# Kernel tuning notes

Hardware: AMD Instinct MI355X
Metric: run time of the kernel (lower is better)

Reference implementation:

```python
import jax, jax.numpy as jnp
import numpy as np

N = 100000
E = 1600000
F_IN = 128
H1, C1 = 8, 8          # conv1: heads=8, hidden_channels=8 -> concat dim 64
H2, C2 = 1, 40         # conv2: heads=1, out=num_classes=40, concat=False
NEG_SLOPE = 0.2
EPS = 1e-16


def setup_inputs() -> dict:
    key = jax.random.key(0)
    ks = jax.random.split(key, 10)
    x = jax.random.normal(ks[0], (N, F_IN), dtype=jnp.float32)
    edge_index = jax.random.randint(ks[1], (2, E), 0, N, dtype=jnp.int32)
    s1 = 1.0 / np.sqrt(F_IN)
    s2 = 1.0 / np.sqrt(H1 * C1)
    W1 = jax.random.normal(ks[2], (F_IN, H1 * C1), dtype=jnp.float32) * s1
    att_src1 = jax.random.normal(ks[3], (H1, C1), dtype=jnp.float32) * s2
    att_dst1 = jax.random.normal(ks[4], (H1, C1), dtype=jnp.float32) * s2
    b1 = jnp.zeros((H1 * C1,), dtype=jnp.float32)
    W2 = jax.random.normal(ks[5], (H1 * C1, H2 * C2), dtype=jnp.float32) * s2
    att_src2 = jax.random.normal(ks[6], (H2, C2), dtype=jnp.float32) * (1.0 / np.sqrt(C2))
    att_dst2 = jax.random.normal(ks[7], (H2, C2), dtype=jnp.float32) * (1.0 / np.sqrt(C2))
    b2 = jnp.zeros((C2,), dtype=jnpp_zeros_dtype()) if False else jnp.zeros((C2,), dtype=jnp.float32)
    return {"x": x, "W1": W1, "att_src1": att_src1, "att_dst1": att_dst1, "b1": b1,
            "W2": W2, "att_src2": att_src2, "att_dst2": att_dst2, "b2": b2,
            "edge_index": edge_index}


def _gat_conv(x, W, att_src, att_dst, bias, src, dst, num_nodes, concat):
    """PyG GATConv (eval mode, self-loops already added to src/dst)."""
    H, C = att_src.shape
    h = (x @ W).reshape(num_nodes, H, C)                 # [N, H, C]
    a_src = jnp.sum(h * att_src[None], axis=-1)          # [N, H]
    a_dst = jnp.sum(h * att_dst[None], axis=-1)          # [N, H]
    e = a_src[src] + a_dst[dst]                          # [Etot, H]
    e = jax.nn.leaky_relu(e, NEG_SLOPE)
    # segment softmax over incoming edges of each dst node
    e_max = jax.ops.segment_max(e, dst, num_segments=num_nodes)   # [N, H]
    ex = jnp.exp(e - e_max[dst])
    denom = jax.ops.segment_sum(ex, dst, num_segments=num_nodes)  # [N, H]
    alpha = ex / (denom[dst] + EPS)                      # [Etot, H]
    msg = h[src] * alpha[..., None]                      # [Etot, H, C]
    out = jax.ops.segment_sum(msg, dst, num_segments=num_nodes)   # [N, H, C]
    if concat:
        out = out.reshape(num_nodes, H * C)
    else:
        out = out.mean(axis=1)
    return out + bias


def reference(x, W1, att_src1, att_dst1, b1, W2, att_src2, att_dst2, b2, edge_index):
    # add self-loops (PyG GATConv default add_self_loops=True)
    loops = jnp.arange(N, dtype=edge_index.dtype)
    src = jnp.concatenate([edge_index[0], loops])
    dst = jnp.concatenate([edge_index[1], loops])
    # dropout layers are identity in eval mode
    emb = jax.nn.elu(_gat_conv(x, W1, att_src1, att_dst1, b1, src, dst, N, True))
    logits = _gat_conv(emb, W2, att_src2, att_dst2, b2, src, dst, N, False)
    return jax.nn.log_softmax(logits, axis=1), emb


def jnp_zeros_dtype():
    return jnp.float32
```

## Files before the change

### kernel.cpp

```cpp
#include <hip/hip_runtime.h>
#include <hip/hip_fp16.h>
#include <math.h>

#define NN 100000
#define EE 1600000
#define ET (EE + NN)
#define FIN 128
#define D1 64
#define H1 8
#define C1 8
#define C2 40
#define NEG 0.2f
#define EPSV 1e-16f
#define LOG2E 1.4426950408889634f

#define NBKT 196
#define BCAP 10240
#define CHUNK 8192
#define NBB ((ET + CHUNK - 1) / CHUNK)
#define H2S 48

__device__ __forceinline__ void edge_sd(int e, const int* __restrict__ ei, int& s, int& d) {
  if (e < EE) { s = ei[e]; d = ei[EE + e]; }
  else        { s = e - EE; d = s; }
}

__global__ __launch_bounds__(256) void scatter_kernel(const int* __restrict__ ei,
                                                      int* __restrict__ gcur,
                                                      int* __restrict__ ecsr) {
  __shared__ int lh[NBKT], lres[NBKT], lcur[NBKT];
  int t = threadIdx.x;
  if (t < NBKT) { lh[t] = 0; lcur[t] = 0; }
  __syncthreads();
  int e0 = blockIdx.x * CHUNK;
  int e1 = min(e0 + CHUNK, ET);
  for (int e = e0 + t; e < e1; e += 256) {
    int d = (e < EE) ? ei[EE + e] : e - EE;
    atomicAdd(&lh[d >> 9], 1);
  }
  __syncthreads();
  if (t < NBKT && lh[t]) lres[t] = atomicAdd(&gcur[t], lh[t]);
  __syncthreads();
  for (int e = e0 + t; e < e1; e += 256) {
    int s, d; edge_sd(e, ei, s, d);
    int b = d >> 9;
    int lp = atomicAdd(&lcur[b], 1);
    ecsr[b * BCAP + lres[b] + lp] = s | ((d & 511) << 17);
  }
}

__global__ __launch_bounds__(256) void bucket2csr_kernel(const int* __restrict__ gcur,
                                                         int2* __restrict__ rowrng,
                                                         int* __restrict__ ecsr) {
  __shared__ int ebuf[BCAP];
  __shared__ int hist[512];
  __shared__ int sd[256];
  int b = blockIdx.x, t = threadIdx.x;
  int base = b * BCAP;
  int cnt = gcur[b];
  hist[t] = 0; hist[t + 256] = 0;
  __syncthreads();
  for (int i = t; i < cnt; i += 256) {
    int p = ecsr[base + i];
    ebuf[i] = p;
    atomicAdd(&hist[p >> 17], 1);
  }
  __syncthreads();
  int h0 = hist[2 * t], h1 = hist[2 * t + 1], s = h0 + h1;
  sd[t] = s;
  __syncthreads();
  for (int off = 1; off < 256; off <<= 1) {
    int x = sd[t];
    int y = (t >= off) ? sd[t - off] : 0;
    __syncthreads();
    sd[t] = x + y;
    __syncthreads();
  }
  int run = sd[t] - s;
  int g = b * 512 + 2 * t;
  if (g < NN)     rowrng[g]     = make_int2(base + run,      base + run + h0);
  if (g + 1 < NN) rowrng[g + 1] = make_int2(base + run + h0, base + run + h0 + h1);
  hist[2 * t] = run;
  hist[2 * t + 1] = run + h0;
  __syncthreads();
  for (int i = t; i < cnt; i += 256) {
    int p = ebuf[i];
    int pos = atomicAdd(&hist[p >> 17], 1);
    ecsr[base + pos] = p & 0x1FFFF;
  }
}

__global__ __launch_bounds__(256) void gemm1_kernel(
    const float* __restrict__ x, const float* __restrict__ W,
    const float* __restrict__ att_s, const float* __restrict__ att_d,
    __half* __restrict__ h, float* __restrict__ as, float* __restrict__ ad) {
  __shared__ float sW[FIN * D1];
  __shared__ float sx[64 * FIN];
  int t = threadIdx.x;
  int node0 = blockIdx.x * 64;
  {
    const float4* Wg = (const float4*)W;
    float4* sWq = (float4*)sW;
    for (int i = t; i < FIN * D1 / 4; i += 256) sWq[i] = Wg[i];
  }
  for (int idx = t; idx < 64 * 32; idx += 256) {
    int node = idx >> 5, kq = idx & 31;
    float4 v = make_float4(0.f, 0.f, 0.f, 0.f);
    if (node0 + node < NN) v = ((const float4*)x)[(size_t)(node0 + node) * 32 + kq];
    *(float4*)&sx[node * FIN + ((kq * 4 + 4 * (node >> 2)) & 127)] = v;
  }
  __syncthreads();
  int lane = t & 63, wid = t >> 6;
  int ng = lane & 15, cgl = lane >> 4;
  int col0 = wid * 16 + cgl * 4;
  float acc[4][4];
#pragma unroll
  for (int a = 0; a < 4; ++a)
#pragma unroll
    for (int c = 0; c < 4; ++c) acc[a][c] = 0.f;
  for (int kk = 0; kk < FIN; kk += 4) {
    float4 xv[4], wv[4];
#pragma unroll
    for (int a = 0; a < 4; ++a) {
      int node = ng * 4 + a;
      xv[a] = *(const float4*)&sx[node * FIN + ((kk + 4 * (node >> 2)) & 127)];
    }
#pragma unroll
    for (int b = 0; b < 4; ++b) wv[b] = *(const float4*)&sW[(kk + b) * D1 + col0];
#pragma unroll
    for (int a = 0; a < 4; ++a) {
      acc[a][0] = fmaf(xv[a].x, wv[0].x, acc[a][0]);
      acc[a][1] = fmaf(xv[a].x, wv[0].y, acc[a][1]);
      acc[a][2] = fmaf(xv[a].x, wv[0].z, acc[a][2]);
      acc[a][3] = fmaf(xv[a].x, wv[0].w, acc[a][3]);
      acc[a][0] = fmaf(xv[a].y, wv[1].x, acc[a][0]);
      acc[a][1] = fmaf(xv[a].y, wv[1].y, acc[a][1]);
      acc[a][2] = fmaf(xv[a].y, wv[1].z, acc[a][2]);
      acc[a][3] = fmaf(xv[a].y, wv[1].w, acc[a][3]);
      acc[a][0] = fmaf(xv[a].z, wv[2].x, acc[a][0]);
      acc[a][1] = fmaf(xv[a].z, wv[2].y, acc[a][1]);
      acc[a][2] = fmaf(xv[a].z, wv[2].z, acc[a][2]);
      acc[a][3] = fmaf(xv[a].z, wv[2].w, acc[a][3]);
      acc[a][0] = fmaf(xv[a].w, wv[3].x, acc[a][0]);
      acc[a][1] = fmaf(xv[a].w, wv[3].y, acc[a][1]);
      acc[a][2] = fmaf(xv[a].w, wv[3].z, acc[a][2]);
      acc[a][3] = fmaf(xv[a].w, wv[3].w, acc[a][3]);
    }
  }
#pragma unroll
  for (int a = 0; a < 4; ++a) {
    int node = node0 + ng * 4 + a;
    if (node < NN) {
      __half2 p01 = __floats2half2_rn(acc[a][0], acc[a][1]);
      __half2 p23 = __floats2half2_rn(acc[a][2], acc[a][3]);
      __half2* hp = (__half2*)&h[(size_t)node * D1 + col0];
      hp[0] = p01; hp[1] = p23;
    }
  }
  float aw_s[4], aw_d[4];
#pragma unroll
  for (int j = 0; j < 4; ++j) {
    aw_s[j] = att_s[col0 + j] * LOG2E;
    aw_d[j] = att_d[col0 + j] * LOG2E;
  }
#pragma unroll
  for (int a = 0; a < 4; ++a) {
    float ps = acc[a][0]*aw_s[0] + acc[a][1]*aw_s[1] + acc[a][2]*aw_s[2] + acc[a][3]*aw_s[3];
    float pd = acc[a][0]*aw_d[0] + acc[a][1]*aw_d[1] + acc[a][2]*aw_d[2] + acc[a][3]*aw_d[3];
    ps += __shfl_xor(ps, 16, 64);
    pd += __shfl_xor(pd, 16, 64);
    int node = node0 + ng * 4 + a;
    if ((cgl & 1) == 0 && node < NN) {
      int head = 2 * wid + (cgl >> 1);
      as[node * H1 + head] = ps;
      ad[node * H1 + head] = pd;
    }
  }
}

__global__ __launch_bounds__(256) void agg1_kernel(
    const int2* __restrict__ rowrng, const int* __restrict__ csr,
    const float* __restrict__ as, const float* __restrict__ ad,
    const __half* __restrict__ h, const float* __restrict__ b1,
    float* __restrict__ emb) {
  int t = threadIdx.x;
  int lane = t & 63;
  int o = lane >> 3;
  int k = lane & 7;
  int ob = lane & 56;
  int node = blockIdx.x * 32 + (t >> 6) * 8 + o;
  int2 rr = rowrng[node];
  int beg = rr.x, deg = rr.y - rr.x, degm1 = deg - 1;
  float adv = ad[node * H1 + k];
  float den = 0.f;
  float a0=0.f,a1=0.f,a2=0.f,a3=0.f,a4=0.f,a5=0.f,a6=0.f,a7=0.f;
  int sreg = csr[beg + min(k, degm1)];
  for (int i = 0; i < deg; i += 8) {
    int snext = csr[beg + min(i + 8 + k, degm1)];
#pragma unroll
    for (int r = 0; r < 8; ++r) {
      int sj = __shfl(sreg, ob + r, 64);
      uint4 u = *(const uint4*)(h + ((size_t)(uint)sj << 6) + (k << 3));
      float av = as[(uint)sj * 8u + k];
      float xx = av + adv; xx = fmaxf(xx, NEG * xx);
      float e = (i + r < deg) ? exp2f(xx) : 0.f;
      den += e;
      float2 f;
      f = __half22float2(*(__half2*)&u.x); a0 = fmaf(f.x, e, a0); a1 = fmaf(f.y, e, a1);
      f = __half22float2(*(__half2*)&u.y); a2 = fmaf(f.x, e, a2); a3 = fmaf(f.y, e, a3);
      f = __half22float2(*(__half2*)&u.z); a4 = fmaf(f.x, e, a4); a5 = fmaf(f.y, e, a5);
      f = __half22float2(*(__half2*)&u.w); a6 = fmaf(f.x, e, a6); a7 = fmaf(f.y, e, a7);
    }
    sreg = snext;
  }
  float4 bv0 = ((const float4*)b1)[2 * k];
  float4 bv1 = ((const float4*)b1)[2 * k + 1];
  float inv = 1.0f / (den + EPSV);
  float v0 = fmaf(a0, inv, bv0.x), v1 = fmaf(a1, inv, bv0.y);
  float v2 = fmaf(a2, inv, bv0.z), v3 = fmaf(a3, inv, bv0.w);
  float v4 = fmaf(a4, inv, bv1.x), v5 = fmaf(a5, inv, bv1.y);
  float v6 = fmaf(a6, inv, bv1.z), v7 = fmaf(a7, inv, bv1.w);
  v0 = v0 > 0.f ? v0 : expm1f(v0); v1 = v1 > 0.f ? v1 : expm1f(v1);
  v2 = v2 > 0.f ? v2 : expm1f(v2); v3 = v3 > 0.f ? v3 : expm1f(v3);
  v4 = v4 > 0.f ? v4 : expm1f(v4); v5 = v5 > 0.f ? v5 : expm1f(v5);
  v6 = v6 > 0.f ? v6 : expm1f(v6); v7 = v7 > 0.f ? v7 : expm1f(v7);
  float4 s0; s0.x = v0; s0.y = v1; s0.z = v2; s0.w = v3;
  float4 s1; s1.x = v4; s1.y = v5; s1.z = v6; s1.w = v7;
  float* ep = emb + (size_t)node * D1 + (k << 3);
  ((float4*)ep)[0] = s0; ((float4*)ep)[1] = s1;
}

__global__ __launch_bounds__(256) void gemm2_kernel(
    const float* __restrict__ emb, const float* __restrict__ W2,
    const float* __restrict__ att_s, const float* __restrict__ att_d,
    __half* __restrict__ h2, float* __restrict__ ad) {
  __shared__ float sW[D1 * D1];
  __shared__ float se[64 * D1];
  __shared__ float sred_s[64], sred_d[64];
  int t = threadIdx.x;
  int node0 = blockIdx.x * 64;
  for (int i = t; i < D1 * D1; i += 256) {
    int k = i >> 6, c = i & 63;
    sW[i] = (c < C2) ? W2[k * C2 + c] : 0.f;
  }
  for (int idx = t; idx < 64 * 16; idx += 256) {
    int node = idx >> 4, kq = idx & 15;
    float4 v = make_float4(0.f, 0.f, 0.f, 0.f);
    if (node0 + node < NN) v = ((const float4*)emb)[(size_t)(node0 + node) * 16 + kq];
    *(float4*)&se[node * D1 + ((kq * 4 + 4 * (node >> 2)) & 63)] = v;
  }
  if (t < 64) { sred_s[t] = 0.f; sred_d[t] = 0.f; }
  __syncthreads();
  int lane = t & 63, wid = t >> 6;
  int ng = lane & 15, cgl = lane >> 4;
  int col0 = wid * 16 + cgl * 4;
  float acc[4][4];
#pragma unroll
  for (int a = 0; a < 4; ++a)
#pragma unroll
    for (int c = 0; c < 4; ++c) acc[a][c] = 0.f;
  for (int kk = 0; kk < D1; kk += 4) {
    float4 xv[4], wv[4];
#pragma unroll
    for (int a = 0; a < 4; ++a) {
      int node = ng * 4 + a;
      xv[a] = *(const float4*)&se[node * D1 + ((kk + 4 * (node >> 2)) & 63)];
    }
#pragma unroll
    for (int b = 0; b < 4; ++b) wv[b] = *(const float4*)&sW[(kk + b) * D1 + col0];
#pragma unroll
    for (int a = 0; a < 4; ++a) {
      acc[a][0] = fmaf(xv[a].x, wv[0].x, acc[a][0]);
      acc[a][1] = fmaf(xv[a].x, wv[0].y, acc[a][1]);
      acc[a][2] = fmaf(xv[a].x, wv[0].z, acc[a][2]);
      acc[a][3] = fmaf(xv[a].x, wv[0].w, acc[a][3]);
      acc[a][0] = fmaf(xv[a].y, wv[1].x, acc[a][0]);
      acc[a][1] = fmaf(xv[a].y, wv[1].y, acc[a][1]);
      acc[a][2] = fmaf(xv[a].y, wv[1].z, acc[a][2]);
      acc[a][3] = fmaf(xv[a].y, wv[1].w, acc[a][3]);
      acc[a][0] = fmaf(xv[a].z, wv[2].x, acc[a][0]);
      acc[a][1] = fmaf(xv[a].z, wv[2].y, acc[a][1]);
      acc[a][2] = fmaf(xv[a].z, wv[2].z, acc[a][2]);
      acc[a][3] = fmaf(xv[a].z, wv[2].w, acc[a][3]);
      acc[a][0] = fmaf(xv[a].w, wv[3].x, acc[a][0]);
      acc[a][1] = fmaf(xv[a].w, wv[3].y, acc[a][1]);
      acc[a][2] = fmaf(xv[a].w, wv[3].z, acc[a][2]);
      acc[a][3] = fmaf(xv[a].w, wv[3].w, acc[a][3]);
    }
  }
  if (col0 < C2) {
#pragma unroll
    for (int a = 0; a < 4; ++a) {
      int node = node0 + ng * 4 + a;
      if (node < NN) {
        __half2 p01 = __floats2half2_rn(acc[a][0], acc[a][1]);
        __half2 p23 = __floats2half2_rn(acc[a][2], acc[a][3]);
        __half2* hp = (__half2*)&h2[(size_t)node * H2S + col0];
        hp[0] = p01; hp[1] = p23;
      }
    }
    float aw_s[4], aw_d[4];
#pragma unroll
    for (int j = 0; j < 4; ++j) {
      aw_s[j] = att_s[col0 + j] * LOG2E;
      aw_d[j] = att_d[col0 + j] * LOG2E;
    }
#pragma unroll
    for (int a = 0; a < 4; ++a) {
      float ps = acc[a][0]*aw_s[0] + acc[a][1]*aw_s[1] + acc[a][2]*aw_s[2] + acc[a][3]*aw_s[3];
      float pd = acc[a][0]*aw_d[0] + acc[a][1]*aw_d[1] + acc[a][2]*aw_d[2] + acc[a][3]*aw_d[3];
      atomicAdd(&sred_s[ng * 4 + a], ps);
      atomicAdd(&sred_d[ng * 4 + a], pd);
    }
  }
  __syncthreads();
  if (t < 64 && node0 + t < NN) {
    h2[(size_t)(node0 + t) * H2S + 40] = __float2half(sred_s[t]);
    ad[node0 + t] = sred_d[t];
  }
}

__global__ __launch_bounds__(256) void agg2_kernel(
    const int2* __restrict__ rowrng, const int* __restrict__ csr,
    const float* __restrict__ ad, const __half* __restrict__ h2,
    const float* __restrict__ b2, float* __restrict__ out) {
  int t = threadIdx.x;
  int lane = t & 63;
  int o = lane >> 3;
  int k = lane & 7;
  int ob = lane & 56;
  int kc = min(k, 4);
  int node = blockIdx.x * 32 + (t >> 6) * 8 + o;
  int2 rr = rowrng[node];
  int beg = rr.x, deg = rr.y - rr.x, degm1 = deg - 1;
  float adv = ad[node];
  float den = 0.f;
  float a0=0.f,a1=0.f,a2=0.f,a3=0.f,a4=0.f,a5=0.f,a6=0.f,a7=0.f;
  int sreg = csr[beg + min(k, degm1)];
  for (int i = 0; i < deg; i += 8) {
    int snext = csr[beg + min(i + 8 + k, degm1)];
#pragma unroll
    for (int r = 0; r < 8; ++r) {
      int sj = __shfl(sreg, ob + r, 64);
      const __half* rA = h2 + (size_t)(uint)sj * H2S;
      uint4 u = *(const uint4*)(rA + (kc << 3));
      float av = __half2float(rA[40]);
      float xx = av + adv; xx = fmaxf(xx, NEG * xx);
      float e = (i + r < deg) ? exp2f(xx) : 0.f;
      den += e;
      float2 f;
      f = __half22float2(*(__half2*)&u.x); a0 = fmaf(f.x, e, a0); a1 = fmaf(f.y, e, a1);
      f = __half22float2(*(__half2*)&u.y); a2 = fmaf(f.x, e, a2); a3 = fmaf(f.y, e, a3);
      f = __half22float2(*(__half2*)&u.z); a4 = fmaf(f.x, e, a4); a5 = fmaf(f.y, e, a5);
      f = __half22float2(*(__half2*)&u.w); a6 = fmaf(f.x, e, a6); a7 = fmaf(f.y, e, a7);
    }
    sreg = snext;
  }
  float4 bv0 = ((const float4*)b2)[2 * kc];
  float4 bv1 = ((const float4*)b2)[2 * kc + 1];
  float inv = 1.0f / (den + EPSV);
  float v0 = fmaf(a0, inv, bv0.x), v1 = fmaf(a1, inv, bv0.y);
  float v2 = fmaf(a2, inv, bv0.z), v3 = fmaf(a3, inv, bv0.w);
  float v4 = fmaf(a4, inv, bv1.x), v5 = fmaf(a5, inv, bv1.y);
  float v6 = fmaf(a6, inv, bv1.z), v7 = fmaf(a7, inv, bv1.w);
  bool act = (k < 5);
  float m = act ? fmaxf(fmaxf(fmaxf(v0, v1), fmaxf(v2, v3)),
                        fmaxf(fmaxf(v4, v5), fmaxf(v6, v7))) : -INFINITY;
#pragma unroll
  for (int off = 1; off < 8; off <<= 1) m = fmaxf(m, __shfl_xor(m, off, 64));
  float ex = act ? (__expf(v0 - m) + __expf(v1 - m) + __expf(v2 - m) + __expf(v3 - m) +
                    __expf(v4 - m) + __expf(v5 - m) + __expf(v6 - m) + __expf(v7 - m)) : 0.f;
#pragma unroll
  for (int off = 1; off < 8; off <<= 1) ex += __shfl_xor(ex, off, 64);
  if (act) {
    float lls = m + logf(ex);
    float4 s0; s0.x = v0 - lls; s0.y = v1 - lls; s0.z = v2 - lls; s0.w = v3 - lls;
    float4 s1; s1.x = v4 - lls; s1.y = v5 - lls; s1.z = v6 - lls; s1.w = v7 - lls;
    float* op = out + (size_t)node * C2 + (k << 3);
    ((float4*)op)[0] = s0; ((float4*)op)[1] = s1;
  }
}

extern "C" void kernel_launch(void* const* d_in, const int* in_sizes, int n_in,
                              void* d_out, int out_size, void* d_ws, size_t ws_size,
                              hipStream_t stream) {
  const float* x    = (const float*)d_in[0];
  const float* W1   = (const float*)d_in[1];
  const float* as1w = (const float*)d_in[2];
  const float* ad1w = (const float*)d_in[3];
  const float* b1   = (const float*)d_in[4];
  const float* W2   = (const float*)d_in[5];
  const float* as2w = (const float*)d_in[6];
  const float* ad2w = (const float*)d_in[7];
  const float* b2   = (const float*)d_in[8];
  const int*   ei   = (const int*)d_in[9];

  float* out   = (float*)d_out;
  float* outls = out;
  float* emb   = out + (long)NN * C2;

  char* wsb = (char*)d_ws;
  __half* h1   = (__half*)wsb; wsb += sizeof(__half) * (size_t)NN * D1;
  __half* h2   = (__half*)wsb; wsb += sizeof(__half) * ((size_t)NN * H2S + 64);
  float* asrc1 = (float*)wsb; wsb += sizeof(float) * (size_t)NN * H1;
  float* adst1 = (float*)wsb; wsb += sizeof(float) * (size_t)NN * H1;
  float* adst2 = (float*)wsb; wsb += sizeof(float) * (size_t)NN;
  int2* rowrng = (int2*)wsb;  wsb += sizeof(int2) * (size_t)NN;
  int* gcur    = (int*)wsb;   wsb += sizeof(int) * (NBKT + 4);
  int* ecsr    = (int*)wsb;   wsb += sizeof(int) * (size_t)NBKT * BCAP;

  hipMemsetAsync(gcur, 0, sizeof(int) * (NBKT + 4), stream);
  scatter_kernel<<<NBB, 256, 0, stream>>>(ei, gcur, ecsr);
  bucket2csr_kernel<<<NBKT, 256, 0, stream>>>(gcur, rowrng, ecsr);

  gemm1_kernel<<<(NN + 63) / 64, 256, 0, stream>>>(x, W1, as1w, ad1w, h1, asrc1, adst1);
  agg1_kernel<<<NN / 32, 256, 0, stream>>>(rowrng, ecsr, asrc1, adst1, h1, b1, emb);

  gemm2_kernel<<<(NN + 63) / 64, 256, 0, stream>>>(emb, W2, as2w, ad2w, h2, adst2);
  agg2_kernel<<<NN / 32, 256, 0, stream>>>(rowrng, ecsr, adst2, h2, b2, outls);
}
```

Before: 316.8 us.

## Use MFMA fp16 GEMMs with folded attention weights and double-buffered gathers

```diff
diff --git a/kernel.cpp b/kernel.cpp
--- a/kernel.cpp
+++ b/kernel.cpp
@@ -18,7 +18,9 @@
 #define BCAP 10240
 #define CHUNK 8192
 #define NBB ((ET + CHUNK - 1) / CHUNK)
-#define H2S 48
+
+typedef _Float16 f16x8 __attribute__((ext_vector_type(8)));
+typedef float f32x4 __attribute__((ext_vector_type(4)));
 
 __device__ __forceinline__ void edge_sd(int e, const int* __restrict__ ei, int& s, int& d) {
   if (e < EE) { s = ei[e]; d = ei[EE + e]; }
@@ -90,128 +92,142 @@
   }
 }
 
+__global__ __launch_bounds__(256) void prep_kernel(
+    const float* __restrict__ W1, const float* __restrict__ as1, const float* __restrict__ ad1,
+    const float* __restrict__ W2, const float* __restrict__ as2, const float* __restrict__ ad2w,
+    __half* __restrict__ Wf1, __half* __restrict__ Wf2) {
+  int gid = blockIdx.x * 256 + threadIdx.x;
+  int stride = gridDim.x * 256;
+  for (int idx = gid; idx < 4 * 5 * 64 * 8; idx += stride) {
+    int j = idx & 7, l = (idx >> 3) & 63;
+    int g = idx >> 9;
+    int ct = g % 5, kk = g / 5;
+    int kdim = kk * 32 + (l >> 4) * 8 + j;
+    int c = l & 15;
+    float v;
+    if (ct < 4) v = W1[kdim * 64 + ct * 16 + c];
+    else {
+      const float* aw = (c < 8) ? as1 : ad1;
+      int hh = c & 7;
+      float acc = 0.f;
+      for (int q = 0; q < 8; ++q) acc += W1[kdim * 64 + hh * 8 + q] * aw[hh * 8 + q];
+      v = acc * LOG2E;
+    }
+    Wf1[idx] = __float2half(v);
+  }
+  for (int idx = gid; idx < 2 * 3 * 64 * 8; idx += stride) {
+    int j = idx & 7, l = (idx >> 3) & 63;
+    int g = idx >> 9;
+    int ct = g % 3, kk = g / 3;
+    int kdim = kk * 32 + (l >> 4) * 8 + j;
+    int c = ct * 16 + (l & 15);
+    float v = 0.f;
+    if (c < C2) v = W2[kdim * C2 + c];
+    else if (c == 40 || c == 41) {
+      const float* aw = (c == 40) ? as2 : ad2w;
+      float acc = 0.f;
+      for (int q = 0; q < C2; ++q) acc += W2[kdim * C2 + q] * aw[q];
+      v = acc * LOG2E;
+    }
+    Wf2[idx] = __float2half(v);
+  }
+}
+
 __global__ __launch_bounds__(256) void gemm1_kernel(
-    const float* __restrict__ x, const float* __restrict__ W,
-    const float* __restrict__ att_s, const float* __restrict__ att_d,
-    __half* __restrict__ h, float* __restrict__ as, float* __restrict__ ad) {
-  __shared__ float sW[FIN * D1];
-  __shared__ float sx[64 * FIN];
+    const float* __restrict__ x, const __half* __restrict__ Wf1,
+    __half* __restrict__ h, __half* __restrict__ as_h, float* __restrict__ ad) {
   int t = threadIdx.x;
-  int node0 = blockIdx.x * 64;
-  {
-    const float4* Wg = (const float4*)W;
-    float4* sWq = (float4*)sW;
-    for (int i = t; i < FIN * D1 / 4; i += 256) sWq[i] = Wg[i];
-  }
-  for (int idx = t; idx < 64 * 32; idx += 256) {
-    int node = idx >> 5, kq = idx & 31;
-    float4 v = make_float4(0.f, 0.f, 0.f, 0.f);
-    if (node0 + node < NN) v = ((const float4*)x)[(size_t)(node0 + node) * 32 + kq];
-    *(float4*)&sx[node * FIN + ((kq * 4 + 4 * (node >> 2)) & 127)] = v;
-  }
-  __syncthreads();
-  int lane = t & 63, wid = t >> 6;
-  int ng = lane & 15, cgl = lane >> 4;
-  int col0 = wid * 16 + cgl * 4;
-  float acc[4][4];
-#pragma unroll
-  for (int a = 0; a < 4; ++a)
-#pragma unroll
-    for (int c = 0; c < 4; ++c) acc[a][c] = 0.f;
-  for (int kk = 0; kk < FIN; kk += 4) {
-    float4 xv[4], wv[4];
-#pragma unroll
-    for (int a = 0; a < 4; ++a) {
-      int node = ng * 4 + a;
-      xv[a] = *(const float4*)&sx[node * FIN + ((kk + 4 * (node >> 2)) & 127)];
-    }
-#pragma unroll
-    for (int b = 0; b < 4; ++b) wv[b] = *(const float4*)&sW[(kk + b) * D1 + col0];
-#pragma unroll
-    for (int a = 0; a < 4; ++a) {
-      acc[a][0] = fmaf(xv[a].x, wv[0].x, acc[a][0]);
-      acc[a][1] = fmaf(xv[a].x, wv[0].y, acc[a][1]);
-      acc[a][2] = fmaf(xv[a].x, wv[0].z, acc[a][2]);
-      acc[a][3] = fmaf(xv[a].x, wv[0].w, acc[a][3]);
-      acc[a][0] = fmaf(xv[a].y, wv[1].x, acc[a][0]);
-      acc[a][1] = fmaf(xv[a].y, wv[1].y, acc[a][1]);
-      acc[a][2] = fmaf(xv[a].y, wv[1].z, acc[a][2]);
-      acc[a][3] = fmaf(xv[a].y, wv[1].w, acc[a][3]);
-      acc[a][0] = fmaf(xv[a].z, wv[2].x, acc[a][0]);
-      acc[a][1] = fmaf(xv[a].z, wv[2].y, acc[a][1]);
-      acc[a][2] = fmaf(xv[a].z, wv[2].z, acc[a][2]);
-      acc[a][3] = fmaf(xv[a].z, wv[2].w, acc[a][3]);
-      acc[a][0] = fmaf(xv[a].w, wv[3].x, acc[a][0]);
-      acc[a][1] = fmaf(xv[a].w, wv[3].y, acc[a][1]);
-      acc[a][2] = fmaf(xv[a].w, wv[3].z, acc[a][2]);
-      acc[a][3] = fmaf(xv[a].w, wv[3].w, acc[a][3]);
-    }
-  }
-#pragma unroll
-  for (int a = 0; a < 4; ++a) {
-    int node = node0 + ng * 4 + a;
-    if (node < NN) {
-      __half2 p01 = __floats2half2_rn(acc[a][0], acc[a][1]);
-      __half2 p23 = __floats2half2_rn(acc[a][2], acc[a][3]);
-      __half2* hp = (__half2*)&h[(size_t)node * D1 + col0];
-      hp[0] = p01; hp[1] = p23;
-    }
-  }
-  float aw_s[4], aw_d[4];
-#pragma unroll
-  for (int j = 0; j < 4; ++j) {
-    aw_s[j] = att_s[col0 + j] * LOG2E;
-    aw_d[j] = att_d[col0 + j] * LOG2E;
-  }
-#pragma unroll
-  for (int a = 0; a < 4; ++a) {
-    float ps = acc[a][0]*aw_s[0] + acc[a][1]*aw_s[1] + acc[a][2]*aw_s[2] + acc[a][3]*aw_s[3];
-    float pd = acc[a][0]*aw_d[0] + acc[a][1]*aw_d[1] + acc[a][2]*aw_d[2] + acc[a][3]*aw_d[3];
-    ps += __shfl_xor(ps, 16, 64);
-    pd += __shfl_xor(pd, 16, 64);
-    int node = node0 + ng * 4 + a;
-    if ((cgl & 1) == 0 && node < NN) {
-      int head = 2 * wid + (cgl >> 1);
-      as[node * H1 + head] = ps;
-      ad[node * H1 + head] = pd;
-    }
-  }
-}
+  int w = t >> 6, lane = t & 63;
+  int col = lane & 15, kg = lane >> 4;
+  int node0 = blockIdx.x * 64 + w * 16;
+  int nodeA = min(node0 + col, NN - 1);
+  const float* xr = x + (size_t)nodeA * FIN + kg * 8;
+  const f16x8* Wq = (const f16x8*)Wf1;
+  f32x4 acc0 = {0.f,0.f,0.f,0.f}, acc1 = acc0, acc2 = acc0, acc3 = acc0, acc4 = acc0;
+#pragma unroll
+  for (int kk = 0; kk < 4; ++kk) {
+    float4 xa = *(const float4*)(xr + kk * 32);
+    float4 xb = *(const float4*)(xr + kk * 32 + 4);
+    f16x8 a;
+    a[0] = (_Float16)xa.x; a[1] = (_Float16)xa.y; a[2] = (_Float16)xa.z; a[3] = (_Float16)xa.w;
+    a[4] = (_Float16)xb.x; a[5] = (_Float16)xb.y; a[6] = (_Float16)xb.z; a[7] = (_Float16)xb.w;
+    acc0 = __builtin_amdgcn_mfma_f32_16x16x32_f16(a, Wq[(kk * 5 + 0) * 64 + lane], acc0, 0, 0, 0);
+    acc1 = __builtin_amdgcn_mfma_f32_16x16x32_f16(a, Wq[(kk * 5 + 1) * 64 + lane], acc1, 0, 0, 0);
+    acc2 = __builtin_amdgcn_mfma_f32_16x16x32_f16(a, Wq[(kk * 5 + 2) * 64 + lane], acc2, 0, 0, 0);
+    acc3 = __builtin_amdgcn_mfma_f32_16x16x32_f16(a, Wq[(kk * 5 + 3) * 64 + lane], acc3, 0, 0, 0);
+    acc4 = __builtin_amdgcn_mfma_f32_16x16x32_f16(a, Wq[(kk * 5 + 4) * 64 + lane], acc4, 0, 0, 0);
+  }
+#pragma unroll
+  for (int reg = 0; reg < 4; ++reg) {
+    int nr = node0 + kg * 4 + reg;
+    if (nr < NN) {
+      h[(size_t)nr * 64 +  0 + col] = __float2half(acc0[reg]);
+      h[(size_t)nr * 64 + 16 + col] = __float2half(acc1[reg]);
+      h[(size_t)nr * 64 + 32 + col] = __float2half(acc2[reg]);
+      h[(size_t)nr * 64 + 48 + col] = __float2half(acc3[reg]);
+      float v = acc4[reg];
+      if (col < 8) as_h[nr * 8 + col] = __float2half(v);
+      else         ad[nr * 8 + col - 8] = v;
+    }
+  }
+}
+
+#define CONS(u, avh, valid) do { \
+    float xx = __half2float(avh) + adv; xx = fmaxf(xx, NEG * xx); \
+    float e = (valid) ? exp2f(xx) : 0.f; den += e; \
+    float2 f; \
+    f = __half22float2(*(const __half2*)&(u).x); a0 = fmaf(f.x, e, a0); a1 = fmaf(f.y, e, a1); \
+    f = __half22float2(*(const __half2*)&(u).y); a2 = fmaf(f.x, e, a2); a3 = fmaf(f.y, e, a3); \
+    f = __half22float2(*(const __half2*)&(u).z); a4 = fmaf(f.x, e, a4); a5 = fmaf(f.y, e, a5); \
+    f = __half22float2(*(const __half2*)&(u).w); a6 = fmaf(f.x, e, a6); a7 = fmaf(f.y, e, a7); \
+  } while (0)
 
 __global__ __launch_bounds__(256) void agg1_kernel(
     const int2* __restrict__ rowrng, const int* __restrict__ csr,
-    const float* __restrict__ as, const float* __restrict__ ad,
+    const __half* __restrict__ as_h, const float* __restrict__ ad,
     const __half* __restrict__ h, const float* __restrict__ b1,
     float* __restrict__ emb) {
   int t = threadIdx.x;
   int lane = t & 63;
-  int o = lane >> 3;
-  int k = lane & 7;
-  int ob = lane & 56;
+  int o = lane >> 3, k = lane & 7, ob = lane & 56;
   int node = blockIdx.x * 32 + (t >> 6) * 8 + o;
   int2 rr = rowrng[node];
   int beg = rr.x, deg = rr.y - rr.x, degm1 = deg - 1;
-  float adv = ad[node * H1 + k];
+  float adv = ad[node * 8 + k];
   float den = 0.f;
   float a0=0.f,a1=0.f,a2=0.f,a3=0.f,a4=0.f,a5=0.f,a6=0.f,a7=0.f;
-  int sreg = csr[beg + min(k, degm1)];
-  for (int i = 0; i < deg; i += 8) {
-    int snext = csr[beg + min(i + 8 + k, degm1)];
+  uint4 uA[8]; __half vA[8]; int sjA[8];
+  int sA = csr[beg + min(k, degm1)];
+#pragma unroll
+  for (int r = 0; r < 8; ++r) sjA[r] = __shfl(sA, ob + r, 64);
+#pragma unroll
+  for (int r = 0; r < 8; ++r) {
+    uA[r] = *(const uint4*)(h + ((size_t)(uint)sjA[r] << 6) + (k << 3));
+    vA[r] = as_h[(uint)sjA[r] * 8u + k];
+  }
+  for (int i = 0; i < deg; i += 16) {
+    int sB = csr[beg + min(i + 8 + k, degm1)];
+    int sjB[8];
+#pragma unroll
+    for (int r = 0; r < 8; ++r) sjB[r] = __shfl(sB, ob + r, 64);
+    uint4 uB[8]; __half vB[8];
 #pragma unroll
     for (int r = 0; r < 8; ++r) {
-      int sj = __shfl(sreg, ob + r, 64);
-      uint4 u = *(const uint4*)(h + ((size_t)(uint)sj << 6) + (k << 3));
-      float av = as[(uint)sj * 8u + k];
-      float xx = av + adv; xx = fmaxf(xx, NEG * xx);
-      float e = (i + r < deg) ? exp2f(xx) : 0.f;
-      den += e;
-      float2 f;
-      f = __half22float2(*(__half2*)&u.x); a0 = fmaf(f.x, e, a0); a1 = fmaf(f.y, e, a1);
-      f = __half22float2(*(__half2*)&u.y); a2 = fmaf(f.x, e, a2); a3 = fmaf(f.y, e, a3);
-      f = __half22float2(*(__half2*)&u.z); a4 = fmaf(f.x, e, a4); a5 = fmaf(f.y, e, a5);
-      f = __half22float2(*(__half2*)&u.w); a6 = fmaf(f.x, e, a6); a7 = fmaf(f.y, e, a7);
-    }
-    sreg = snext;
+      uB[r] = *(const uint4*)(h + ((size_t)(uint)sjB[r] << 6) + (k << 3));
+      vB[r] = as_h[(uint)sjB[r] * 8u + k];
+    }
+#pragma unroll
+    for (int r = 0; r < 8; ++r) CONS(uA[r], vA[r], i + r < deg);
+    int sA2 = csr[beg + min(i + 16 + k, degm1)];
+#pragma unroll
+    for (int r = 0; r < 8; ++r) sjA[r] = __shfl(sA2, ob + r, 64);
+#pragma unroll
+    for (int r = 0; r < 8; ++r) {
+      uA[r] = *(const uint4*)(h + ((size_t)(uint)sjA[r] << 6) + (k << 3));
+      vA[r] = as_h[(uint)sjA[r] * 8u + k];
+    }
+#pragma unroll
+    for (int r = 0; r < 8; ++r) CONS(uB[r], vB[r], i + 8 + r < deg);
   }
   float4 bv0 = ((const float4*)b1)[2 * k];
   float4 bv1 = ((const float4*)b1)[2 * k + 1];
@@ -231,92 +247,38 @@
 }
 
 __global__ __launch_bounds__(256) void gemm2_kernel(
-    const float* __restrict__ emb, const float* __restrict__ W2,
-    const float* __restrict__ att_s, const float* __restrict__ att_d,
-    __half* __restrict__ h2, float* __restrict__ ad) {
-  __shared__ float sW[D1 * D1];
-  __shared__ float se[64 * D1];
-  __shared__ float sred_s[64], sred_d[64];
+    const float* __restrict__ emb, const __half* __restrict__ Wf2,
+    __half* __restrict__ h2, float* __restrict__ ad2) {
   int t = threadIdx.x;
-  int node0 = blockIdx.x * 64;
-  for (int i = t; i < D1 * D1; i += 256) {
-    int k = i >> 6, c = i & 63;
-    sW[i] = (c < C2) ? W2[k * C2 + c] : 0.f;
-  }
-  for (int idx = t; idx < 64 * 16; idx += 256) {
-    int node = idx >> 4, kq = idx & 15;
-    float4 v = make_float4(0.f, 0.f, 0.f, 0.f);
-    if (node0 + node < NN) v = ((const float4*)emb)[(size_t)(node0 + node) * 16 + kq];
-    *(float4*)&se[node * D1 + ((kq * 4 + 4 * (node >> 2)) & 63)] = v;
-  }
-  if (t < 64) { sred_s[t] = 0.f; sred_d[t] = 0.f; }
-  __syncthreads();
-  int lane = t & 63, wid = t >> 6;
-  int ng = lane & 15, cgl = lane >> 4;
-  int col0 = wid * 16 + cgl * 4;
-  float acc[4][4];
-#pragma unroll
-  for (int a = 0; a < 4; ++a)
-#pragma unroll
-    for (int c = 0; c < 4; ++c) acc[a][c] = 0.f;
-  for (int kk = 0; kk < D1; kk += 4) {
-    float4 xv[4], wv[4];
-#pragma unroll
-    for (int a = 0; a < 4; ++a) {
-      int node = ng * 4 + a;
-      xv[a] = *(const float4*)&se[node * D1 + ((kk + 4 * (node >> 2)) & 63)];
-    }
-#pragma unroll
-    for (int b = 0; b < 4; ++b) wv[b] = *(const float4*)&sW[(kk + b) * D1 + col0];
-#pragma unroll
-    for (int a = 0; a < 4; ++a) {
-      acc[a][0] = fmaf(xv[a].x, wv[0].x, acc[a][0]);
-      acc[a][1] = fmaf(xv[a].x, wv[0].y, acc[a][1]);
-      acc[a][2] = fmaf(xv[a].x, wv[0].z, acc[a][2]);
-      acc[a][3] = fmaf(xv[a].x, wv[0].w, acc[a][3]);
-      acc[a][0] = fmaf(xv[a].y, wv[1].x, acc[a][0]);
-      acc[a][1] = fmaf(xv[a].y, wv[1].y, acc[a][1]);
-      acc[a][2] = fmaf(xv[a].y, wv[1].z, acc[a][2]);
-      acc[a][3] = fmaf(xv[a].y, wv[1].w, acc[a][3]);
-      acc[a][0] = fmaf(xv[a].z, wv[2].x, acc[a][0]);
-      acc[a][1] = fmaf(xv[a].z, wv[2].y, acc[a][1]);
-      acc[a][2] = fmaf(xv[a].z, wv[2].z, acc[a][2]);
-      acc[a][3] = fmaf(xv[a].z, wv[2].w, acc[a][3]);
-      acc[a][0] = fmaf(xv[a].w, wv[3].x, acc[a][0]);
-      acc[a][1] = fmaf(xv[a].w, wv[3].y, acc[a][1]);
-      acc[a][2] = fmaf(xv[a].w, wv[3].z, acc[a][2]);
-      acc[a][3] = fmaf(xv[a].w, wv[3].w, acc[a][3]);
-    }
-  }
-  if (col0 < C2) {
-#pragma unroll
-    for (int a = 0; a < 4; ++a) {
-      int node = node0 + ng * 4 + a;
-      if (node < NN) {
-        __half2 p01 = __floats2half2_rn(acc[a][0], acc[a][1]);
-        __half2 p23 = __floats2half2_rn(acc[a][2], acc[a][3]);
-        __half2* hp = (__half2*)&h2[(size_t)node * H2S + col0];
-        hp[0] = p01; hp[1] = p23;
-      }
-    }
-    float aw_s[4], aw_d[4];
-#pragma unroll
-    for (int j = 0; j < 4; ++j) {
-      aw_s[j] = att_s[col0 + j] * LOG2E;
-      aw_d[j] = att_d[col0 + j] * LOG2E;
-    }
-#pragma unroll
-    for (int a = 0; a < 4; ++a) {
-      float ps = acc[a][0]*aw_s[0] + acc[a][1]*aw_s[1] + acc[a][2]*aw_s[2] + acc[a][3]*aw_s[3];
-      float pd = acc[a][0]*aw_d[0] + acc[a][1]*aw_d[1] + acc[a][2]*aw_d[2] + acc[a][3]*aw_d[3];
-      atomicAdd(&sred_s[ng * 4 + a], ps);
-      atomicAdd(&sred_d[ng * 4 + a], pd);
-    }
-  }
-  __syncthreads();
-  if (t < 64 && node0 + t < NN) {
-    h2[(size_t)(node0 + t) * H2S + 40] = __float2half(sred_s[t]);
-    ad[node0 + t] = sred_d[t];
+  int w = t >> 6, lane = t & 63;
+  int col = lane & 15, kg = lane >> 4;
+  int node0 = blockIdx.x * 64 + w * 16;
+  int nodeA = min(node0 + col, NN - 1);
+  const float* er = emb + (size_t)nodeA * D1 + kg * 8;
+  const f16x8* Wq = (const f16x8*)Wf2;
+  f32x4 acc0 = {0.f,0.f,0.f,0.f}, acc1 = acc0, acc2 = acc0;
+#pragma unroll
+  for (int kk = 0; kk < 2; ++kk) {
+    float4 xa = *(const float4*)(er + kk * 32);
+    float4 xb = *(const float4*)(er + kk * 32 + 4);
+    f16x8 a;
+    a[0] = (_Float16)xa.x; a[1] = (_Float16)xa.y; a[2] = (_Float16)xa.z; a[3] = (_Float16)xa.w;
+    a[4] = (_Float16)xb.x; a[5] = (_Float16)xb.y; a[6] = (_Float16)xb.z; a[7] = (_Float16)xb.w;
+    acc0 = __builtin_amdgcn_mfma_f32_16x16x32_f16(a, Wq[(kk * 3 + 0) * 64 + lane], acc0, 0, 0, 0);
+    acc1 = __builtin_amdgcn_mfma_f32_16x16x32_f16(a, Wq[(kk * 3 + 1) * 64 + lane], acc1, 0, 0, 0);
+    acc2 = __builtin_amdgcn_mfma_f32_16x16x32_f16(a, Wq[(kk * 3 + 2) * 64 + lane], acc2, 0, 0, 0);
+  }
+#pragma unroll
+  for (int reg = 0; reg < 4; ++reg) {
+    int nr = node0 + kg * 4 + reg;
+    if (nr < NN) {
+      h2[(size_t)nr * 64 +  0 + col] = __float2half(acc0[reg]);
+      h2[(size_t)nr * 64 + 16 + col] = __float2half(acc1[reg]);
+      float v = acc2[reg];
+      if (col < 8)       h2[(size_t)nr * 64 + 32 + col] = __float2half(v);
+      else if (col == 8) h2[(size_t)nr * 64 + 40] = __float2half(v);
+      else if (col == 9) ad2[nr] = v;
+    }
   }
 }
 
@@ -326,9 +288,7 @@
     const float* __restrict__ b2, float* __restrict__ out) {
   int t = threadIdx.x;
   int lane = t & 63;
-  int o = lane >> 3;
-  int k = lane & 7;
-  int ob = lane & 56;
+  int o = lane >> 3, k = lane & 7, ob = lane & 56;
   int kc = min(k, 4);
   int node = blockIdx.x * 32 + (t >> 6) * 8 + o;
   int2 rr = rowrng[node];
@@ -336,25 +296,41 @@
   float adv = ad[node];
   float den = 0.f;
   float a0=0.f,a1=0.f,a2=0.f,a3=0.f,a4=0.f,a5=0.f,a6=0.f,a7=0.f;
-  int sreg = csr[beg + min(k, degm1)];
-  for (int i = 0; i < deg; i += 8) {
-    int snext = csr[beg + min(i + 8 + k, degm1)];
+  uint4 uA[8]; __half vA[8]; int sjA[8];
+  int sA = csr[beg + min(k, degm1)];
+#pragma unroll
+  for (int r = 0; r < 8; ++r) sjA[r] = __shfl(sA, ob + r, 64);
+#pragma unroll
+  for (int r = 0; r < 8; ++r) {
+    const __half* rp = h2 + ((size_t)(uint)sjA[r] << 6);
+    uA[r] = *(const uint4*)(rp + (kc << 3));
+    vA[r] = rp[40];
+  }
+  for (int i = 0; i < deg; i += 16) {
+    int sB = csr[beg + min(i + 8 + k, degm1)];
+    int sjB[8];
+#pragma unroll
+    for (int r = 0; r < 8; ++r) sjB[r] = __shfl(sB, ob + r, 64);
+    uint4 uB[8]; __half vB[8];
 #pragma unroll
     for (int r = 0; r < 8; ++r) {
-      int sj = __shfl(sreg, ob + r, 64);
-      const __half* rA = h2 + (size_t)(uint)sj * H2S;
-      uint4 u = *(const uint4*)(rA + (kc << 3));
-      float av = __half2float(rA[40]);
-      float xx = av + adv; xx = fmaxf(xx, NEG * xx);
-      float e = (i + r < deg) ? exp2f(xx) : 0.f;
-      den += e;
-      float2 f;
-      f = __half22float2(*(__half2*)&u.x); a0 = fmaf(f.x, e, a0); a1 = fmaf(f.y, e, a1);
-      f = __half22float2(*(__half2*)&u.y); a2 = fmaf(f.x, e, a2); a3 = fmaf(f.y, e, a3);
-      f = __half22float2(*(__half2*)&u.z); a4 = fmaf(f.x, e, a4); a5 = fmaf(f.y, e, a5);
-      f = __half22float2(*(__half2*)&u.w); a6 = fmaf(f.x, e, a6); a7 = fmaf(f.y, e, a7);
-    }
-    sreg = snext;
+      const __half* rp = h2 + ((size_t)(uint)sjB[r] << 6);
+      uB[r] = *(const uint4*)(rp + (kc << 3));
+      vB[r] = rp[40];
+    }
+#pragma unroll
+    for (int r = 0; r < 8; ++r) CONS(uA[r], vA[r], i + r < deg);
+    int sA2 = csr[beg + min(i + 16 + k, degm1)];
+#pragma unroll
+    for (int r = 0; r < 8; ++r) sjA[r] = __shfl(sA2, ob + r, 64);
+#pragma unroll
+    for (int r = 0; r < 8; ++r) {
+      const __half* rp = h2 + ((size_t)(uint)sjA[r] << 6);
+      uA[r] = *(const uint4*)(rp + (kc << 3));
+      vA[r] = rp[40];
+    }
+#pragma unroll
+    for (int r = 0; r < 8; ++r) CONS(uB[r], vB[r], i + 8 + r < deg);
   }
   float4 bv0 = ((const float4*)b2)[2 * kc];
   float4 bv1 = ((const float4*)b2)[2 * kc + 1];
@@ -401,21 +377,24 @@
 
   char* wsb = (char*)d_ws;
   __half* h1   = (__half*)wsb; wsb += sizeof(__half) * (size_t)NN * D1;
-  __half* h2   = (__half*)wsb; wsb += sizeof(__half) * ((size_t)NN * H2S + 64);
-  float* asrc1 = (float*)wsb; wsb += sizeof(float) * (size_t)NN * H1;
+  __half* h2   = (__half*)wsb; wsb += sizeof(__half) * ((size_t)NN * 64 + 64);
+  __half* ash1 = (__half*)wsb; wsb += sizeof(__half) * (size_t)NN * H1;
   float* adst1 = (float*)wsb; wsb += sizeof(float) * (size_t)NN * H1;
   float* adst2 = (float*)wsb; wsb += sizeof(float) * (size_t)NN;
   int2* rowrng = (int2*)wsb;  wsb += sizeof(int2) * (size_t)NN;
   int* gcur    = (int*)wsb;   wsb += sizeof(int) * (NBKT + 4);
+  __half* Wf1  = (__half*)wsb; wsb += sizeof(__half) * 4 * 5 * 64 * 8;
+  __half* Wf2  = (__half*)wsb; wsb += sizeof(__half) * 2 * 3 * 64 * 8;
   int* ecsr    = (int*)wsb;   wsb += sizeof(int) * (size_t)NBKT * BCAP;
 
+  prep_kernel<<<16, 256, 0, stream>>>(W1, as1w, ad1w, W2, as2w, ad2w, Wf1, Wf2);
   hipMemsetAsync(gcur, 0, sizeof(int) * (NBKT + 4), stream);
   scatter_kernel<<<NBB, 256, 0, stream>>>(ei, gcur, ecsr);
   bucket2csr_kernel<<<NBKT, 256, 0, stream>>>(gcur, rowrng, ecsr);
 
-  gemm1_kernel<<<(NN + 63) / 64, 256, 0, stream>>>(x, W1, as1w, ad1w, h1, asrc1, adst1);
-  agg1_kernel<<<NN / 32, 256, 0, stream>>>(rowrng, ecsr, asrc1, adst1, h1, b1, emb);
-
-  gemm2_kernel<<<(NN + 63) / 64, 256, 0, stream>>>(emb, W2, as2w, ad2w, h2, adst2);
+  gemm1_kernel<<<(NN + 63) / 64, 256, 0, stream>>>(x, Wf1, h1, ash1, adst1);
+  agg1_kernel<<<NN / 32, 256, 0, stream>>>(rowrng, ecsr, ash1, adst1, h1, b1, emb);
+
+  gemm2_kernel<<<(NN + 63) / 64, 256, 0, stream>>>(emb, Wf2, h2, adst2);
   agg2_kernel<<<NN / 32, 256, 0, stream>>>(rowrng, ecsr, adst2, h2, b2, outls);
 }
```

Result: faster. 264.7 us (-16.4%).
